# Optimization experiments

Measured on AMD Instinct MI355X. Metric: run time of the kernel, lower is better.

The kernel has to match this reference:

```python
import jax, jax.numpy as jnp
import numpy as np
from jax import lax

LAYER_NUM = 5
ITER_NUM = 10


def setup_inputs() -> dict:
    key = jax.random.key(0)
    ks = jax.random.split(key, 5)
    x = jax.random.normal(ks[0], (32, 1, 512, 512), dtype=jnp.float32)
    Wx = jax.random.normal(ks[1], (LAYER_NUM, 1, 1, 5, 5), dtype=jnp.float32) * 0.1
    bx = jax.random.normal(ks[2], (LAYER_NUM,), dtype=jnp.float32) * 0.1
    Wy = jax.random.normal(ks[3], (LAYER_NUM, 1, 1, 5, 5), dtype=jnp.float32) * 0.1
    by = jax.random.normal(ks[4], (LAYER_NUM,), dtype=jnp.float32) * 0.1
    return {"x": x, "Wx": Wx, "bx": bx, "Wy": Wy, "by": by}


def _conv5x5(z, w, b):
    # z: [B,1,H,W], w: [1,1,5,5], b: scalar; 'same' padding of 2
    out = lax.conv_general_dilated(
        z, w, window_strides=(1, 1), padding=((2, 2), (2, 2)),
        dimension_numbers=("NCHW", "OIHW", "NCHW"))
    return out + b


def reference(x, Wx, bx, Wy, by):
    # normalize_tensor_0to1: global min-max normalization
    x = (x - jnp.min(x)) / (jnp.max(x) - jnp.min(x))
    y = x
    for _ in range(ITER_NUM):
        for l in range(LAYER_NUM):
            x = jax.nn.relu(_conv5x5(x, Wx[l], bx[l]) + _conv5x5(y, Wy[l], by[l]))
        # normalize_tensor_sumto1: divide by global sum
        x = x / jnp.sum(x)
    return x
```

## Files before the change

### kernel.cpp

```cpp
#include <hip/hip_runtime.h>
#include <hip/hip_fp16.h>

#define HW    512
#define NPIX  (HW*HW)
#define IMGS  32
#define NTOT  (IMGS*NPIX)

#define TLW 64
#define TLH 32
#define SW  84
#define SH  52
#define SA  84

#define PT  64
#define PS  68

typedef float v2f __attribute__((ext_vector_type(2)));
typedef float v4f __attribute__((ext_vector_type(4)));

__device__ __forceinline__ float wave_reduce_sum(float v) {
    #pragma unroll
    for (int off = 32; off > 0; off >>= 1) v += __shfl_down(v, off);
    return v;
}

__device__ __forceinline__ float2 h2tof2(unsigned u) {
    __half2 h = *reinterpret_cast<const __half2*>(&u);
    return __half22float2(h);
}

__global__ __launch_bounds__(256) void minmax_partial(
    const float4* __restrict__ x, float* __restrict__ pmin, float* __restrict__ pmax)
{
    const int n4 = NTOT / 4;
    int tid = threadIdx.x + blockIdx.x * 256;
    int stride = gridDim.x * 256;
    float mn = 3.402823466e38f, mx = -3.402823466e38f;
    for (int i = tid; i < n4; i += stride) {
        float4 v = x[i];
        mn = fminf(mn, fminf(fminf(v.x, v.y), fminf(v.z, v.w)));
        mx = fmaxf(mx, fmaxf(fmaxf(v.x, v.y), fmaxf(v.z, v.w)));
    }
    #pragma unroll
    for (int off = 32; off > 0; off >>= 1) {
        mn = fminf(mn, __shfl_down(mn, off));
        mx = fmaxf(mx, __shfl_down(mx, off));
    }
    __shared__ float smn[4], smx[4];
    int lane = threadIdx.x & 63, wid = threadIdx.x >> 6;
    if (lane == 0) { smn[wid] = mn; smx[wid] = mx; }
    __syncthreads();
    if (threadIdx.x == 0) {
        mn = fminf(fminf(smn[0], smn[1]), fminf(smn[2], smn[3]));
        mx = fmaxf(fmaxf(smx[0], smx[1]), fmaxf(smx[2], smx[3]));
        pmin[blockIdx.x] = mn;
        pmax[blockIdx.x] = mx;
    }
}

__global__ __launch_bounds__(256) void minmax_final(
    const float* __restrict__ pmin, const float* __restrict__ pmax,
    float* __restrict__ scal, int nparts)
{
    float mn = 3.402823466e38f, mx = -3.402823466e38f;
    for (int i = threadIdx.x; i < nparts; i += 256) {
        mn = fminf(mn, pmin[i]);
        mx = fmaxf(mx, pmax[i]);
    }
    #pragma unroll
    for (int off = 32; off > 0; off >>= 1) {
        mn = fminf(mn, __shfl_down(mn, off));
        mx = fmaxf(mx, __shfl_down(mx, off));
    }
    __shared__ float smn[4], smx[4];
    int lane = threadIdx.x & 63, wid = threadIdx.x >> 6;
    if (lane == 0) { smn[wid] = mn; smx[wid] = mx; }
    __syncthreads();
    if (threadIdx.x == 0) {
        mn = fminf(fminf(smn[0], smn[1]), fminf(smn[2], smn[3]));
        mx = fmaxf(fmaxf(smx[0], smx[1]), fmaxf(smx[2], smx[3]));
        scal[0] = mn;
        scal[1] = 1.0f / (mx - mn);
    }
}

__global__ __launch_bounds__(256) void normalize_k(
    const float4* __restrict__ x, float4* __restrict__ y, const float* __restrict__ scal)
{
    const int n4 = NTOT / 4;
    float mn = scal[0], inv = scal[1];
    int tid = threadIdx.x + blockIdx.x * 256;
    int stride = gridDim.x * 256;
    for (int i = tid; i < n4; i += stride) {
        float4 v = x[i];
        v.x = (v.x - mn) * inv;
        v.y = (v.y - mn) * inv;
        v.z = (v.z - mn) * inv;
        v.w = (v.w - mn) * inv;
        y[i] = v;
    }
}

__global__ __launch_bounds__(256) void prep(
    const float* __restrict__ x, const float* __restrict__ scal,
    const float* __restrict__ bx,
    const float* __restrict__ Wy, const float* __restrict__ by,
    __half* __restrict__ y16, __half* __restrict__ Yc)
{
    __shared__ __align__(16) float ys[PS * PS];

    const int img = blockIdx.z;
    const int tileX = blockIdx.x * PT;
    const int tileY = blockIdx.y * PT;
    const int tid = threadIdx.x;
    const float mn = scal[0], inv = scal[1];
    const float* xim = x + (size_t)img * NPIX;

    for (int p = tid; p < PS * PS / 2; p += 256) {
        int row = p / (PS / 2);
        int cp  = p - row * (PS / 2);
        int gr = tileY - 2 + row;
        int gc = tileX - 2 + 2 * cp;
        float a = 0.f, b = 0.f;
        if (((unsigned)gr < HW) & ((unsigned)gc < HW)) {
            float2 v = *(const float2*)(xim + (size_t)gr * HW + gc);
            a = (v.x - mn) * inv;
            b = (v.y - mn) * inv;
        }
        ys[row * PS + 2 * cp]     = a;
        ys[row * PS + 2 * cp + 1] = b;
    }
    __syncthreads();

    for (int p = tid; p < PT * PT / 2; p += 256) {
        int row = p / (PT / 2);
        int cp  = p - row * (PT / 2);
        float2 v = *(const float2*)&ys[(row + 2) * PS + 2 * cp + 2];
        *(__half2*)(y16 + (size_t)img * NPIX + (size_t)(tileY + row) * HW + tileX + 2 * cp)
            = __floats2half2_rn(v.x, v.y);
    }

    const int br = tid >> 4, bc = tid & 15;
    const float* yp = ys + (4 * br) * PS + 4 * bc;

    #pragma unroll
    for (int l = 0; l < 5; ++l) {
        float w[25];
        #pragma unroll
        for (int k = 0; k < 25; ++k) w[k] = Wy[25 * l + k];
        const float bias = bx[l] + by[l];

        float acc[4][4] = {};
        #pragma unroll
        for (int di = 0; di < 8; ++di) {
            float xr[8];
            *(float4*)&xr[0] = *(const float4*)(yp + di * PS);
            *(float4*)&xr[4] = *(const float4*)(yp + di * PS + 4);
            #pragma unroll
            for (int o = 0; o < 4; ++o) {
                const int ki = di - o;
                if (ki >= 0 && ki <= 4) {
                    #pragma unroll
                    for (int kj = 0; kj < 5; ++kj) {
                        const float wa = w[ki * 5 + kj];
                        #pragma unroll
                        for (int j = 0; j < 4; ++j)
                            acc[o][j] = fmaf(xr[kj + j], wa, acc[o][j]);
                    }
                }
            }
        }
        __half* yl = Yc + (size_t)l * NTOT + (size_t)img * NPIX;
        #pragma unroll
        for (int o = 0; o < 4; ++o) {
            __half2* q = (__half2*)(yl + (size_t)(tileY + 4 * br + o) * HW + tileX + 4 * bc);
            q[0] = __floats2half2_rn(acc[o][0] + bias, acc[o][1] + bias);
            q[1] = __floats2half2_rn(acc[o][2] + bias, acc[o][3] + bias);
        }
    }
}

template<int WIN, int HIN, int L, bool LAST>
__device__ __forceinline__ float conv_layer_yc(
    const float* __restrict__ inb, float* __restrict__ outb,
    const float* __restrict__ Wx,
    const unsigned (&ycA)[5][4], const unsigned (&ycB)[5][4],
    __half* __restrict__ hout, float* __restrict__ fout,
    int img, int tileX, int tileY)
{
    constexpr int WOUT = WIN - 4, HOUT = HIN - 4;
    constexpr int NBC = WOUT / 4, NBR = HOUT / 4, NB = NBC * NBR;
    const int tid = threadIdx.x;
    float bsum = 0.0f;
    if (tid < NB) {
        float w[25];
        #pragma unroll
        for (int k = 0; k < 25; ++k) w[k] = Wx[25 * L + k];

        const int br = tid / NBC, bc = tid - (tid / NBC) * NBC;
        const float* xp = inb + (4 * br) * SA + 4 * bc;

        v2f acc2[4][2] = {};
        #pragma unroll
        for (int di = 0; di < 8; ++di) {
            const v4f a0 = *(const v4f*)(xp + di * SA);
            const v4f a1 = *(const v4f*)(xp + di * SA + 4);
            v2f pr[7];
            pr[0] = __builtin_shufflevector(a0, a0, 0, 1);
            pr[1] = __builtin_shufflevector(a0, a0, 1, 2);
            pr[2] = __builtin_shufflevector(a0, a0, 2, 3);
            pr[3] = __builtin_shufflevector(a0, a1, 3, 4);
            pr[4] = __builtin_shufflevector(a1, a1, 0, 1);
            pr[5] = __builtin_shufflevector(a1, a1, 1, 2);
            pr[6] = __builtin_shufflevector(a1, a1, 2, 3);
            #pragma unroll
            for (int o = 0; o < 4; ++o) {
                const int ki = di - o;
                if (ki >= 0 && ki <= 4) {
                    #pragma unroll
                    for (int kj = 0; kj < 5; ++kj) {
                        const float ww = w[ki * 5 + kj];
                        v2f w2; w2.x = ww; w2.y = ww;
                        acc2[o][0] = __builtin_elementwise_fma(pr[kj],     w2, acc2[o][0]);
                        acc2[o][1] = __builtin_elementwise_fma(pr[kj + 2], w2, acc2[o][1]);
                    }
                }
            }
        }

        const int gy0 = tileY - 8 + 2 * L + 4 * br;
        const int gx0 = tileX - 8 + 2 * L + 4 * bc;

        if constexpr (LAST) {
            const size_t base = (size_t)img * NPIX;
            #pragma unroll
            for (int o = 0; o < 4; ++o) {
                float2 u = h2tof2(ycA[L][o]);
                float2 t = h2tof2(ycB[L][o]);
                float4 v;
                v.x = fmaxf(acc2[o][0].x + u.x, 0.0f);
                v.y = fmaxf(acc2[o][0].y + u.y, 0.0f);
                v.z = fmaxf(acc2[o][1].x + t.x, 0.0f);
                v.w = fmaxf(acc2[o][1].y + t.y, 0.0f);
                const size_t idx = base + (size_t)(gy0 + o) * HW + gx0;
                if (fout) {
                    *(float4*)(fout + idx) = v;
                } else {
                    __half2* q = (__half2*)(hout + idx);
                    q[0] = __floats2half2_rn(v.x, v.y);
                    q[1] = __floats2half2_rn(v.z, v.w);
                }
                bsum += (v.x + v.y) + (v.z + v.w);
            }
        } else {
            bool cok[4];
            #pragma unroll
            for (int j = 0; j < 4; ++j) cok[j] = (unsigned)(gx0 + j) < HW;
            #pragma unroll
            for (int o = 0; o < 4; ++o) {
                const bool rok = (unsigned)(gy0 + o) < HW;
                float2 u = h2tof2(ycA[L][o]);
                float2 t = h2tof2(ycB[L][o]);
                v4f v;
                v.x = (rok && cok[0]) ? fmaxf(acc2[o][0].x + u.x, 0.0f) : 0.0f;
                v.y = (rok && cok[1]) ? fmaxf(acc2[o][0].y + u.y, 0.0f) : 0.0f;
                v.z = (rok && cok[2]) ? fmaxf(acc2[o][1].x + t.x, 0.0f) : 0.0f;
                v.w = (rok && cok[3]) ? fmaxf(acc2[o][1].y + t.y, 0.0f) : 0.0f;
                *(v4f*)(outb + (4 * br + o) * SA + 4 * bc) = v;
            }
        }
    }
    (void)img;
    return bsum;
}

__global__ __launch_bounds__(256, 4) void fused5_yc(
    const __half* __restrict__ xin, const float* __restrict__ Wx,
    const __half* __restrict__ Ych, const float* __restrict__ sum_prev,
    __half* __restrict__ hout, float* __restrict__ fout,
    float* __restrict__ sum_out)
{
    __shared__ __align__(16) float Xa[SA * SH];
    __shared__ __align__(16) float Xb[SA * (SH - 4)];

    const int img = blockIdx.z;
    const int tileX = blockIdx.x * TLW;
    const int tileY = blockIdx.y * TLH;
    const int tid = threadIdx.x;

    const float scale = sum_prev ? (1.0f / sum_prev[0]) : 1.0f;
    const __half* xim = xin + (size_t)img * NPIX;
    const __half* ycb = Ych + (size_t)img * NPIX;
    const size_t PL = (size_t)IMGS * NPIX;

    constexpr int NPAIR = SW * SH / 2;
    for (int p = tid; p < NPAIR; p += 256) {
        int row = p / (SW / 2);
        int cp  = p - row * (SW / 2);
        int gr = tileY - 10 + row;
        int gc = tileX - 10 + 2 * cp;
        unsigned u = 0u;
        if (((unsigned)gr < HW) & ((unsigned)gc < HW))
            u = *(const unsigned*)(xim + (size_t)gr * HW + gc);
        float2 f = h2tof2(u);
        v2f fv; fv.x = f.x * scale; fv.y = f.y * scale;
        *(v2f*)&Xa[2 * p] = fv;
    }

    unsigned ycA[5][4], ycB[5][4];
    {
        const int NBCs[5] = {20, 19, 18, 17, 16};
        #pragma unroll
        for (int l = 0; l < 5; ++l) {
            const int br = tid / NBCs[l], bc = tid - br * NBCs[l];
            const int gy0 = tileY - 8 + 2 * l + 4 * br;
            const int gx0 = tileX - 8 + 2 * l + 4 * bc;
            const __half* pl = ycb + (ptrdiff_t)l * PL;
            #pragma unroll
            for (int o = 0; o < 4; ++o) {
                const __half* p = pl + (ptrdiff_t)(gy0 + o) * HW + gx0;
                ycA[l][o] = *(const unsigned*)(p);
                ycB[l][o] = *(const unsigned*)(p + 2);
            }
        }
    }
    __syncthreads();

    conv_layer_yc<84, 52, 0, false>(Xa, Xb, Wx, ycA, ycB, nullptr, nullptr, img, tileX, tileY);
    __syncthreads();
    conv_layer_yc<80, 48, 1, false>(Xb, Xa, Wx, ycA, ycB, nullptr, nullptr, img, tileX, tileY);
    __syncthreads();
    conv_layer_yc<76, 44, 2, false>(Xa, Xb, Wx, ycA, ycB, nullptr, nullptr, img, tileX, tileY);
    __syncthreads();
    conv_layer_yc<72, 40, 3, false>(Xb, Xa, Wx, ycA, ycB, nullptr, nullptr, img, tileX, tileY);
    __syncthreads();
    float bs = conv_layer_yc<68, 36, 4, true>(Xa, nullptr, Wx, ycA, ycB, hout, fout, img, tileX, tileY);

    bs = wave_reduce_sum(bs);
    __shared__ float ssum[4];
    if ((tid & 63) == 0) ssum[tid >> 6] = bs;
    __syncthreads();
    if (tid == 0)
        atomicAdd(sum_out, (ssum[0] + ssum[1]) + (ssum[2] + ssum[3]));
}

__global__ __launch_bounds__(256) void final_scale_raw(
    float4* __restrict__ io, const float* __restrict__ sum9)
{
    const int n4 = NTOT / 4;
    const float s = 1.0f / sum9[0];
    int tid = threadIdx.x + blockIdx.x * 256;
    int stride = gridDim.x * 256;
    for (int i = tid; i < n4; i += stride) {
        float4 v = io[i];
        v.x *= s; v.y *= s; v.z *= s; v.w *= s;
        io[i] = v;
    }
}

template<int WIN, int HIN, int L, bool LAST>
__device__ __forceinline__ float conv_layer(
    const float* __restrict__ inb, float* __restrict__ outb,
    const float* __restrict__ yb,
    const float* __restrict__ Wx, const float* __restrict__ Wy,
    const float* __restrict__ bx, const float* __restrict__ by,
    float* __restrict__ gout, int img, int tileX, int tileY)
{
    constexpr int WOUT = WIN - 4, HOUT = HIN - 4;
    constexpr int NBC = WOUT / 4, NBR = HOUT / 4, NB = NBC * NBR;
    const int tid = threadIdx.x;
    float bsum = 0.0f;
    if (tid < NB) {
        float wxl[25], wyl[25];
        #pragma unroll
        for (int k = 0; k < 25; ++k) {
            wxl[k] = Wx[25 * L + k];
            wyl[k] = Wy[25 * L + k];
        }
        const float bias = bx[L] + by[L];
        const int br = tid / NBC, bc = tid - (tid / NBC) * NBC;
        const float* xp = inb + (4 * br) * WIN + 4 * bc;
        const float* yp = yb + (4 * br + 2 * L) * 84 + 4 * bc + 2 * L;

        float acc[4][4] = {};
        #pragma unroll
        for (int di = 0; di < 8; ++di) {
            float xr[8], yr[8];
            *(float4*)&xr[0] = *(const float4*)(xp + di * WIN);
            *(float4*)&xr[4] = *(const float4*)(xp + di * WIN + 4);
            if constexpr ((L & 1) == 0) {
                *(float4*)&yr[0] = *(const float4*)(yp + di * 84);
                *(float4*)&yr[4] = *(const float4*)(yp + di * 84 + 4);
            } else {
                *(float2*)&yr[0] = *(const float2*)(yp + di * 84);
                *(float4*)&yr[2] = *(const float4*)(yp + di * 84 + 2);
                *(float2*)&yr[6] = *(const float2*)(yp + di * 84 + 6);
            }
            #pragma unroll
            for (int o = 0; o < 4; ++o) {
                const int ki = di - o;
                if (ki >= 0 && ki <= 4) {
                    #pragma unroll
                    for (int kj = 0; kj < 5; ++kj) {
                        const float wa = wxl[ki * 5 + kj];
                        const float wb = wyl[ki * 5 + kj];
                        #pragma unroll
                        for (int j = 0; j < 4; ++j)
                            acc[o][j] = fmaf(xr[kj + j], wa,
                                        fmaf(yr[kj + j], wb, acc[o][j]));
                    }
                }
            }
        }

        if constexpr (LAST) {
            #pragma unroll
            for (int o = 0; o < 4; ++o) {
                float4 v;
                v.x = fmaxf(acc[o][0] + bias, 0.0f);
                v.y = fmaxf(acc[o][1] + bias, 0.0f);
                v.z = fmaxf(acc[o][2] + bias, 0.0f);
                v.w = fmaxf(acc[o][3] + bias, 0.0f);
                float* g = gout + (size_t)img * NPIX +
                           (size_t)(tileY + 4 * br + o) * HW + tileX + 4 * bc;
                *(float4*)g = v;
                bsum += (v.x + v.y) + (v.z + v.w);
            }
        } else {
            const int gy0 = tileY - 8 + 2 * L + 4 * br;
            const int gx0 = tileX - 8 + 2 * L + 4 * bc;
            bool cok[4];
            #pragma unroll
            for (int j = 0; j < 4; ++j) cok[j] = (unsigned)(gx0 + j) < HW;
            #pragma unroll
            for (int o = 0; o < 4; ++o) {
                const bool rok = (unsigned)(gy0 + o) < HW;
                float4 v;
                v.x = (rok && cok[0]) ? fmaxf(acc[o][0] + bias, 0.0f) : 0.0f;
                v.y = (rok && cok[1]) ? fmaxf(acc[o][1] + bias, 0.0f) : 0.0f;
                v.z = (rok && cok[2]) ? fmaxf(acc[o][2] + bias, 0.0f) : 0.0f;
                v.w = (rok && cok[3]) ? fmaxf(acc[o][3] + bias, 0.0f) : 0.0f;
                *(float4*)(outb + (4 * br + o) * WOUT + 4 * bc) = v;
            }
        }
    }
    (void)img; (void)gout;
    return bsum;
}

__global__ __launch_bounds__(256, 3) void fused5(
    const float* __restrict__ xin, const float* __restrict__ yin,
    const float* __restrict__ Wx, const float* __restrict__ bx,
    const float* __restrict__ Wy, const float* __restrict__ by,
    const float* __restrict__ scale_p,
    float* __restrict__ gout, float* __restrict__ spart)
{
    __shared__ __align__(16) float Xa[84 * 52];
    __shared__ __align__(16) float Xb[80 * 48];
    __shared__ __align__(16) float Yb[84 * 52];

    const int img = blockIdx.z;
    const int tileX = blockIdx.x * TLW;
    const int tileY = blockIdx.y * TLH;
    const int tid = threadIdx.x;

    const float scale = scale_p ? scale_p[0] : 1.0f;
    const float* xim = xin + (size_t)img * NPIX;
    const float* yim = yin + (size_t)img * NPIX;

    constexpr int NPAIR = 84 * 52 / 2;
    for (int p = tid; p < NPAIR; p += 256) {
        int row = p / 42;
        int cp  = p - row * 42;
        int gr = tileY - 10 + row;
        int gc = tileX - 10 + 2 * cp;
        float2 xv = make_float2(0.f, 0.f), yv = make_float2(0.f, 0.f);
        if (((unsigned)gr < HW) & ((unsigned)gc < HW)) {
            xv = *(const float2*)(xim + (size_t)gr * HW + gc);
            yv = *(const float2*)(yim + (size_t)gr * HW + gc);
        }
        Xa[2 * p]     = xv.x * scale;
        Xa[2 * p + 1] = xv.y * scale;
        *(float2*)&Yb[2 * p] = yv;
    }
    __syncthreads();

    conv_layer<84, 52, 0, false>(Xa, Xb, Yb, Wx, Wy, bx, by, nullptr, img, tileX, tileY);
    __syncthreads();
    conv_layer<80, 48, 1, false>(Xb, Xa, Yb, Wx, Wy, bx, by, nullptr, img, tileX, tileY);
    __syncthreads();
    conv_layer<76, 44, 2, false>(Xa, Xb, Yb, Wx, Wy, bx, by, nullptr, img, tileX, tileY);
    __syncthreads();
    conv_layer<72, 40, 3, false>(Xb, Xa, Yb, Wx, Wy, bx, by, nullptr, img, tileX, tileY);
    __syncthreads();
    float bs = conv_layer<68, 36, 4, true>(Xa, nullptr, Yb, Wx, Wy, bx, by, gout, img, tileX, tileY);

    bs = wave_reduce_sum(bs);
    __shared__ float ssum[4];
    if ((tid & 63) == 0) ssum[tid >> 6] = bs;
    __syncthreads();
    if (tid == 0) {
        int b = (blockIdx.z * gridDim.y + blockIdx.y) * gridDim.x + blockIdx.x;
        spart[b] = (ssum[0] + ssum[1]) + (ssum[2] + ssum[3]);
    }
}

__global__ __launch_bounds__(256) void reduce_sum(
    const float* __restrict__ p, int n, float* __restrict__ invS)
{
    float s = 0.0f;
    for (int i = threadIdx.x; i < n; i += 256) s += p[i];
    s = wave_reduce_sum(s);
    __shared__ float sh[4];
    int lane = threadIdx.x & 63, wid = threadIdx.x >> 6;
    if (lane == 0) sh[wid] = s;
    __syncthreads();
    if (threadIdx.x == 0) invS[0] = 1.0f / ((sh[0] + sh[1]) + (sh[2] + sh[3]));
}

__global__ __launch_bounds__(256) void final_scale(
    float4* __restrict__ io, const float* __restrict__ invS)
{
    const int n4 = NTOT / 4;
    const float s = invS[0];
    int tid = threadIdx.x + blockIdx.x * 256;
    int stride = gridDim.x * 256;
    for (int i = tid; i < n4; i += stride) {
        float4 v = io[i];
        v.x *= s; v.y *= s; v.z *= s; v.w *= s;
        io[i] = v;
    }
}

extern "C" void kernel_launch(void* const* d_in, const int* in_sizes, int n_in,
                              void* d_out, int out_size, void* d_ws, size_t ws_size,
                              hipStream_t stream)
{
    const float* x  = (const float*)d_in[0];
    const float* Wx = (const float*)d_in[1];
    const float* bx = (const float*)d_in[2];
    const float* Wy = (const float*)d_in[3];
    const float* by = (const float*)d_in[4];
    float* out = (float*)d_out;
    float* ws  = (float*)d_ws;

    float* sums  = ws;
    float* scal  = ws + 12;
    float* invS  = ws + 16;
    float* pmin  = ws + 64;
    float* pmax  = ws + 64 + 1024;
    float* spart = ws + 4096;
    __half* y16 = (__half*)(ws + 16384);
    __half* xhA = y16 + NTOT;
    __half* xhB = xhA + NTOT;
    __half* Ych = xhB + NTOT;

    const size_t needYC = ((size_t)16384 + 4ull * NTOT + 16384) * sizeof(float);

    minmax_partial<<<1024, 256, 0, stream>>>((const float4*)x, pmin, pmax);
    minmax_final<<<1, 256, 0, stream>>>(pmin, pmax, scal, 1024);

    if (ws_size >= needYC) {
        hipMemsetAsync(sums, 0, 10 * sizeof(float), stream);

        dim3 pgrid(HW / PT, HW / PT, IMGS);
        prep<<<pgrid, 256, 0, stream>>>(x, scal, bx, Wy, by, y16, Ych);

        dim3 grid(HW / TLW, HW / TLH, IMGS);
        const __half* cur = y16;
        for (int it = 0; it < 10; ++it) {
            __half* hdst = (it % 2 == 0) ? xhA : xhB;
            float* fdst = (it == 9) ? out : nullptr;
            const float* sum_prev = (it > 0) ? (sums + (it - 1)) : nullptr;
            fused5_yc<<<grid, 256, 0, stream>>>(cur, Wx, Ych, sum_prev, hdst, fdst, sums + it);
            cur = hdst;
        }
        final_scale_raw<<<2048, 256, 0, stream>>>((float4*)out, sums + 9);
    } else {
        float* ybuf = ws + 16384;
        float* xAf  = ybuf + NTOT;
        normalize_k<<<2048, 256, 0, stream>>>((const float4*)x, (float4*)ybuf, scal);
        dim3 grid(HW / TLW, HW / TLH, IMGS);
        const float* cur = ybuf;
        for (int it = 0; it < 10; ++it) {
            float* dst = (it % 2 == 0) ? xAf : out;
            const float* scale_p = (it > 0) ? (invS + (it - 1)) : nullptr;
            fused5<<<grid, 256, 0, stream>>>(cur, ybuf, Wx, bx, Wy, by, scale_p, dst, spart);
            reduce_sum<<<1, 256, 0, stream>>>(spart, 4096, invS + it);
            cur = dst;
        }
        final_scale<<<2048, 256, 0, stream>>>((float4*)out, invS + 9);
    }
}
```

Measured before the change: 772.2 us.

## Run fused conv layers in place in one shared buffer to raise occupancy

Drops the ping-pong second shared-memory buffer: each layer reads its input tile into registers, synchronises, then writes its output back into the same buffer and synchronises again. This roughly halves LDS use per block, and the launch bound is raised from 4 to 8 blocks per multiprocessor to use the room. The cost is an extra barrier per layer, plus register pressure under the tighter launch bound, since the ycA/ycB arrays and accumulators must now fit in fewer registers.

After: 1.093 ms. +41.5%, slower.

```diff
diff --git a/kernel.cpp b/kernel.cpp
--- a/kernel.cpp
+++ b/kernel.cpp
@@ -181,9 +181,8 @@
 }
 
 template<int WIN, int HIN, int L, bool LAST>
-__device__ __forceinline__ float conv_layer_yc(
-    const float* __restrict__ inb, float* __restrict__ outb,
-    const float* __restrict__ Wx,
+__device__ __forceinline__ float conv_layer_ip(
+    float* __restrict__ buf, const float* __restrict__ Wx,
     const unsigned (&ycA)[5][4], const unsigned (&ycB)[5][4],
     __half* __restrict__ hout, float* __restrict__ fout,
     int img, int tileX, int tileY)
@@ -191,16 +190,17 @@
     constexpr int WOUT = WIN - 4, HOUT = HIN - 4;
     constexpr int NBC = WOUT / 4, NBR = HOUT / 4, NB = NBC * NBR;
     const int tid = threadIdx.x;
-    float bsum = 0.0f;
-    if (tid < NB) {
+    const bool active = tid < NB;
+    const int br = active ? (tid / NBC) : 0;
+    const int bc = active ? (tid - br * NBC) : 0;
+
+    v2f acc2[4][2] = {};
+    if (active) {
         float w[25];
         #pragma unroll
         for (int k = 0; k < 25; ++k) w[k] = Wx[25 * L + k];
 
-        const int br = tid / NBC, bc = tid - (tid / NBC) * NBC;
-        const float* xp = inb + (4 * br) * SA + 4 * bc;
-
-        v2f acc2[4][2] = {};
+        const float* xp = buf + (4 * br) * SA + 4 * bc;
         #pragma unroll
         for (int di = 0; di < 8; ++di) {
             const v4f a0 = *(const v4f*)(xp + di * SA);
@@ -227,10 +227,15 @@
                 }
             }
         }
-
-        const int gy0 = tileY - 8 + 2 * L + 4 * br;
-        const int gx0 = tileX - 8 + 2 * L + 4 * bc;
-
+    }
+
+    if constexpr (!LAST) __syncthreads();
+
+    const int gy0 = tileY - 8 + 2 * L + 4 * br;
+    const int gx0 = tileX - 8 + 2 * L + 4 * bc;
+
+    float bsum = 0.0f;
+    if (active) {
         if constexpr (LAST) {
             const size_t base = (size_t)img * NPIX;
             #pragma unroll
@@ -266,22 +271,23 @@
                 v.y = (rok && cok[1]) ? fmaxf(acc2[o][0].y + u.y, 0.0f) : 0.0f;
                 v.z = (rok && cok[2]) ? fmaxf(acc2[o][1].x + t.x, 0.0f) : 0.0f;
                 v.w = (rok && cok[3]) ? fmaxf(acc2[o][1].y + t.y, 0.0f) : 0.0f;
-                *(v4f*)(outb + (4 * br + o) * SA + 4 * bc) = v;
-            }
-        }
-    }
+                *(v4f*)(buf + (4 * br + o) * SA + 4 * bc) = v;
+            }
+        }
+    }
+
+    if constexpr (!LAST) __syncthreads();
     (void)img;
     return bsum;
 }
 
-__global__ __launch_bounds__(256, 4) void fused5_yc(
+__global__ __launch_bounds__(256, 8) void fused5_yc(
     const __half* __restrict__ xin, const float* __restrict__ Wx,
     const __half* __restrict__ Ych, const float* __restrict__ sum_prev,
     __half* __restrict__ hout, float* __restrict__ fout,
     float* __restrict__ sum_out)
 {
     __shared__ __align__(16) float Xa[SA * SH];
-    __shared__ __align__(16) float Xb[SA * (SH - 4)];
 
     const int img = blockIdx.z;
     const int tileX = blockIdx.x * TLW;
@@ -326,15 +332,11 @@
     }
     __syncthreads();
 
-    conv_layer_yc<84, 52, 0, false>(Xa, Xb, Wx, ycA, ycB, nullptr, nullptr, img, tileX, tileY);
-    __syncthreads();
-    conv_layer_yc<80, 48, 1, false>(Xb, Xa, Wx, ycA, ycB, nullptr, nullptr, img, tileX, tileY);
-    __syncthreads();
-    conv_layer_yc<76, 44, 2, false>(Xa, Xb, Wx, ycA, ycB, nullptr, nullptr, img, tileX, tileY);
-    __syncthreads();
-    conv_layer_yc<72, 40, 3, false>(Xb, Xa, Wx, ycA, ycB, nullptr, nullptr, img, tileX, tileY);
-    __syncthreads();
-    float bs = conv_layer_yc<68, 36, 4, true>(Xa, nullptr, Wx, ycA, ycB, hout, fout, img, tileX, tileY);
+    conv_layer_ip<84, 52, 0, false>(Xa, Wx, ycA, ycB, nullptr, nullptr, img, tileX, tileY);
+    conv_layer_ip<80, 48, 1, false>(Xa, Wx, ycA, ycB, nullptr, nullptr, img, tileX, tileY);
+    conv_layer_ip<76, 44, 2, false>(Xa, Wx, ycA, ycB, nullptr, nullptr, img, tileX, tileY);
+    conv_layer_ip<72, 40, 3, false>(Xa, Wx, ycA, ycB, nullptr, nullptr, img, tileX, tileY);
+    float bs = conv_layer_ip<68, 36, 4, true>(Xa, Wx, ycA, ycB, hout, fout, img, tileX, tileY);
 
     bs = wave_reduce_sum(bs);
     __shared__ float ssum[4];
```
